# Performance work log

Hardware: AMD Instinct MI355X
Metric: run time of the kernel (lower is better)

Reference implementation:

```python
import jax, jax.numpy as jnp
import numpy as np
from jax import lax

B, T, E, H, V, D_ACT, OUT = 128, 512, 12, 512, 16, 10, 64


def setup_inputs() -> dict:
    key = jax.random.key(0)
    ks = jax.random.split(key, 9)
    ts = jax.random.uniform(ks[0], (B, T, 2), dtype=jnp.float32)
    idx = jax.random.randint(ks[1], (B, T), 0, V).astype(jnp.float32)
    x = jnp.concatenate([ts, idx[..., None]], axis=-1)  # [B,T,3], col2 = activity ids
    emb = jax.random.normal(ks[2], (V, D_ACT), jnp.float32) * 0.1
    emb = emb.at[0].set(0.0)  # padding_idx=0
    W_fwd = jax.random.normal(ks[3], (E, 3 * H), jnp.float32) / np.sqrt(E).astype(np.float32)
    b_fwd = jnp.zeros((3 * H,), jnp.float32)
    W_bwd = jax.random.normal(ks[4], (E, 3 * H), jnp.float32) / np.sqrt(E).astype(np.float32)
    b_bwd = jnp.zeros((3 * H,), jnp.float32)
    weight_Mu = jax.random.normal(ks[5], (2 * H, 1), jnp.float32) * 0.1
    W_out = jax.random.normal(ks[6], (OUT, 2 * H), jnp.float32) * 0.01  # torch Linear layout [out,in]
    b_out = jnp.zeros((OUT,), jnp.float32)
    return {"x": x, "emb": emb, "W_fwd": W_fwd, "b_fwd": b_fwd,
            "W_bwd": W_bwd, "b_bwd": b_bwd, "weight_Mu": weight_Mu,
            "W_out": W_out, "b_out": b_out}


def _fo_pool(z, f):
    # h_t = f_t * h_{t-1} + (1 - f_t) * z_t, scanned over time (axis 0)
    def step(c, zf):
        z_t, f_t = zf
        c = f_t * c + (1.0 - f_t) * z_t
        return c, c
    c0 = jnp.zeros_like(z[0])
    _, cs = lax.scan(step, c0, (z, f))
    return cs  # [T,B,H]


def _qrnn_dir(inp, W, b):
    # inp: [T,B,E] -> gates [T,B,3H]
    Y = inp @ W + b
    Z, F_, O = jnp.split(Y, 3, axis=-1)
    Z = jnp.tanh(Z)
    F_ = jax.nn.sigmoid(F_)
    O = jax.nn.sigmoid(O)
    C = _fo_pool(Z, F_)
    return O * C  # [T,B,H]


def reference(x, emb, W_fwd, b_fwd, W_bwd, b_bwd, weight_Mu, W_out, b_out):
    ts = x[:, :, :2]                                   # [B,T,2] time features
    act = emb[x[:, :, 2].astype(jnp.int32)]            # [B,T,10]
    enc = jnp.concatenate([ts, act], axis=-1)          # [B,T,E]
    inp = jnp.transpose(enc, (1, 0, 2))                # [T,B,E]
    h_f = _qrnn_dir(inp, W_fwd, b_fwd)                 # [T,B,H]
    h_b = _qrnn_dir(inp[::-1], W_bwd, b_bwd)[::-1]     # reverse-direction QRNN
    out = jnp.concatenate([h_f, h_b], axis=-1)         # [T,B,2H]
    out = jax.nn.relu(jnp.transpose(out, (1, 0, 2)))   # [B,T,2H]
    attn = jax.nn.softmax(out @ weight_Mu, axis=1)     # [B,T,1], softmax over time
    context = jnp.einsum('btd,bt->bd', out, attn[..., 0])  # [B,2H]
    context = jax.nn.relu(context)
    return context @ W_out.T + b_out                   # [B,OUT]
```

## Files before the change

kernel.cpp:

```cpp
#include <hip/hip_runtime.h>
#include <hip/hip_bf16.h>

typedef short short8 __attribute__((ext_vector_type(8)));

#define B_   128
#define T_   512
#define H_   512
#define V_   16
#define OUT_ 64
#define DH_  1024

#define SCAN_LDS (V_*H_*16 + T_*16)

__device__ __forceinline__ float bf2f(unsigned short u) {
    union { unsigned int i; float f; } x; x.i = ((unsigned int)u) << 16; return x.f;
}
__device__ __forceinline__ float sigm(float x) {
    return __builtin_amdgcn_rcpf(1.f + __expf(-x));
}

__global__ __launch_bounds__(512) void qrnn_scan2(
    const float* __restrict__ x,
    const float* __restrict__ emb,
    const float* __restrict__ Wf, const float* __restrict__ bf_,
    const float* __restrict__ Wb, const float* __restrict__ bb_,
    __hip_bfloat16* __restrict__ hbuf)
{
    const int b = blockIdx.x, dir = blockIdx.y, h = threadIdx.x;
    const float* __restrict__ W    = dir ? Wb  : Wf;
    const float* __restrict__ bias = dir ? bb_ : bf_;

    extern __shared__ char smem[];
    float4* tab = (float4*)smem;
    float4* tsq = (float4*)(smem + V_*H_*16);

    {
        const int t = h;
        const float* xp = x + ((size_t)b*T_ + t)*3;
        float t0 = xp[0], t1 = xp[1];
        int v = (int)xp[2];
        tsq[t] = make_float4(t0, t1, __int_as_float(v), 0.f);
    }

    float w0[3], w1[3], wt[10][3];
#pragma unroll
    for (int g = 0; g < 3; ++g) {
        w0[g] = W[g*H_ + h];
        w1[g] = W[1536 + g*H_ + h];
#pragma unroll
        for (int e = 0; e < 10; ++e)
            wt[e][g] = W[(2+e)*1536 + g*H_ + h];
    }
    const float bz = bias[h], bfv = bias[H_+h], bov = bias[2*H_+h];

#pragma unroll
    for (int v = 0; v < V_; ++v) {
        float a0 = bz, a1 = bfv, a2 = bov;
#pragma unroll
        for (int e = 0; e < 10; ++e) {
            const float ev = emb[v*10 + e];
            a0 = fmaf(ev, wt[e][0], a0);
            a1 = fmaf(ev, wt[e][1], a1);
            a2 = fmaf(ev, wt[e][2], a2);
        }
        tab[v*H_ + h] = make_float4(a0, a1, a2, 0.f);
    }
    __syncthreads();

    float c = 0.f;
    __hip_bfloat16* hb = hbuf + ((size_t)b*T_ + (dir ? T_-1 : 0))*DH_ + dir*H_ + h;
    const ptrdiff_t stride = dir ? -(ptrdiff_t)DH_ : (ptrdiff_t)DH_;
    int t = dir ? T_-1 : 0;
    const int tstep = dir ? -1 : 1;

#pragma unroll 4
    for (int s = 0; s < T_; ++s) {
        const float4 q = tsq[t];
        const int v = __float_as_int(q.z);
        const float4 g = tab[v*H_ + h];
        float zp = fmaf(q.x, w0[0], fmaf(q.y, w1[0], g.x));
        float fp = fmaf(q.x, w0[1], fmaf(q.y, w1[1], g.y));
        float op = fmaf(q.x, w0[2], fmaf(q.y, w1[2], g.z));
        const float f = sigm(fp);
        const float o = sigm(op);
        const float z = fmaf(2.f, sigm(2.f*zp), -1.f);
        c = fmaf(f, c - z, z);
        const float hv = fmaxf(o * c, 0.f);
        *hb = __float2bfloat16(hv);
        hb += stride; t += tstep;
    }
}

__global__ __launch_bounds__(256) void score2(
    const __hip_bfloat16* __restrict__ hbuf, const float* __restrict__ Mu,
    float* __restrict__ s)
{
    const int row  = blockIdx.x*4 + (threadIdx.x >> 6);
    const int lane = threadIdx.x & 63;
    const short8* hp = (const short8*)(hbuf + (size_t)row*DH_);
    const float4* mp = (const float4*)Mu;
    float acc = 0.f;
#pragma unroll
    for (int k = 0; k < 2; ++k) {
        const int idx = k*64 + lane;
        const short8 hv = hp[idx];
        const float4 m0 = mp[idx*2];
        const float4 m1 = mp[idx*2 + 1];
        acc = fmaf(bf2f((unsigned short)hv[0]), m0.x, acc);
        acc = fmaf(bf2f((unsigned short)hv[1]), m0.y, acc);
        acc = fmaf(bf2f((unsigned short)hv[2]), m0.z, acc);
        acc = fmaf(bf2f((unsigned short)hv[3]), m0.w, acc);
        acc = fmaf(bf2f((unsigned short)hv[4]), m1.x, acc);
        acc = fmaf(bf2f((unsigned short)hv[5]), m1.y, acc);
        acc = fmaf(bf2f((unsigned short)hv[6]), m1.z, acc);
        acc = fmaf(bf2f((unsigned short)hv[7]), m1.w, acc);
    }
#pragma unroll
    for (int off = 32; off; off >>= 1) acc += __shfl_down(acc, off);
    if (lane == 0) s[row] = acc;
}

__global__ __launch_bounds__(512) void softmax_kernel(
    const float* __restrict__ s, float* __restrict__ w)
{
    const int b = blockIdx.x;
    const int t = threadIdx.x;
    const float v = s[b*T_ + t];

    __shared__ float redm[8];
    __shared__ float reds[8];

    float m = v;
#pragma unroll
    for (int off = 32; off; off >>= 1) m = fmaxf(m, __shfl_xor(m, off));
    if ((t & 63) == 0) redm[t >> 6] = m;
    __syncthreads();
    float mall = redm[0];
#pragma unroll
    for (int i = 1; i < 8; ++i) mall = fmaxf(mall, redm[i]);

    const float e = __expf(v - mall);
    float sum = e;
#pragma unroll
    for (int off = 32; off; off >>= 1) sum += __shfl_xor(sum, off);
    if ((t & 63) == 0) reds[t >> 6] = sum;
    __syncthreads();
    float sall = 0.f;
#pragma unroll
    for (int i = 0; i < 8; ++i) sall += reds[i];

    w[b*T_ + t] = e / sall;
}

__global__ __launch_bounds__(256) void context2(
    const __hip_bfloat16* __restrict__ hbuf, const float* __restrict__ w,
    float* __restrict__ ctx)
{
    const int b  = blockIdx.x;
    const int d0 = (blockIdx.y*256 + threadIdx.x)*2;

    __shared__ float ws[T_];
    for (int t = threadIdx.x; t < T_; t += 256) ws[t] = w[b*T_ + t];
    __syncthreads();

    const unsigned int* hp = (const unsigned int*)(hbuf + (size_t)b*T_*DH_ + d0);
    float a0 = 0.f, a1 = 0.f;
#pragma unroll 8
    for (int t = 0; t < T_; ++t) {
        const unsigned int u = hp[(size_t)t*(DH_/2)];
        a0 = fmaf(bf2f((unsigned short)(u & 0xffffu)), ws[t], a0);
        a1 = fmaf(bf2f((unsigned short)(u >> 16)),     ws[t], a1);
    }
    float2* cp = (float2*)(ctx + b*DH_ + d0);
    *cp = make_float2(fmaxf(a0, 0.f), fmaxf(a1, 0.f));
}

__global__ __launch_bounds__(256) void out_kernel(
    const float* __restrict__ ctx, const float* __restrict__ Wout,
    const float* __restrict__ bout, float* __restrict__ out)
{
    const int idx  = blockIdx.x*4 + (threadIdx.x >> 6);
    const int lane = threadIdx.x & 63;
    const int b = idx >> 6;
    const int o = idx & 63;
    const float* cp = ctx + b*DH_;
    const float* wp = Wout + o*DH_;
    float acc = 0.f;
#pragma unroll
    for (int k = 0; k < DH_/64; ++k) {
        const int d = lane + k*64;
        acc = fmaf(cp[d], wp[d], acc);
    }
#pragma unroll
    for (int off = 32; off; off >>= 1) acc += __shfl_down(acc, off);
    if (lane == 0) out[idx] = acc + bout[o];
}

extern "C" void kernel_launch(void* const* d_in, const int* in_sizes, int n_in,
                              void* d_out, int out_size, void* d_ws, size_t ws_size,
                              hipStream_t stream)
{
    const float* x    = (const float*)d_in[0];
    const float* emb  = (const float*)d_in[1];
    const float* Wf   = (const float*)d_in[2];
    const float* bf_  = (const float*)d_in[3];
    const float* Wb   = (const float*)d_in[4];
    const float* bb_  = (const float*)d_in[5];
    const float* Mu   = (const float*)d_in[6];
    const float* Wout = (const float*)d_in[7];
    const float* bout = (const float*)d_in[8];
    float* out = (float*)d_out;

    char* ws = (char*)d_ws;
    const size_t hbytes = (size_t)B_*T_*DH_*sizeof(__hip_bfloat16);
    __hip_bfloat16* hbuf = (__hip_bfloat16*)ws;
    float* s   = (float*)(ws + hbytes);
    float* w   = s + B_*T_;
    float* ctx = w + B_*T_;

    (void)hipFuncSetAttribute((const void*)qrnn_scan2,
                              hipFuncAttributeMaxDynamicSharedMemorySize,
                              SCAN_LDS);

    qrnn_scan2<<<dim3(B_, 2), 512, SCAN_LDS, stream>>>(x, emb, Wf, bf_, Wb, bb_, hbuf);
    score2<<<(B_*T_)/4, 256, 0, stream>>>(hbuf, Mu, s);
    softmax_kernel<<<B_, 512, 0, stream>>>(s, w);
    context2<<<dim3(B_, 2), 256, 0, stream>>>(hbuf, w, ctx);
    out_kernel<<<(B_*OUT_)/4, 256, 0, stream>>>(ctx, Wout, bout, out);
}
```

Measured before the change: 209.7 us.

## Fuse attention score into QRNN scan and split context reduction over time

Each scan step now computes the attention score on the fly: the wave reduces h·Mu with shuffles and atomically adds it into the score buffer, so the separate score kernel and its full re-read of hbuf go away. The scan reads timestep features and vocab ids in packed 8-step groups to cut LDS loads. The context kernel is split into 8 time chunks per batch with atomic accumulation, and the ReLU moves into the output kernel. A zero kernel clears the accumulators first. In exchange, every step now pays for six shuffles plus atomics inside the serial scan loop.

After: 296.4 us. 41.4% more time.

```diff
diff --git a/kernel.cpp b/kernel.cpp
--- a/kernel.cpp
+++ b/kernel.cpp
@@ -1,7 +1,5 @@
 #include <hip/hip_runtime.h>
 #include <hip/hip_bf16.h>
-
-typedef short short8 __attribute__((ext_vector_type(8)));
 
 #define B_   128
 #define T_   512
@@ -10,7 +8,10 @@
 #define OUT_ 64
 #define DH_  1024
 
-#define SCAN_LDS (V_*H_*16 + T_*16)
+#define TAB_BYTES (V_*H_*16)
+#define TSA_BYTES (T_*8)
+#define VPK_BYTES (T_)
+#define SCAN_LDS  (TAB_BYTES + TSA_BYTES + VPK_BYTES)
 
 __device__ __forceinline__ float bf2f(unsigned short u) {
     union { unsigned int i; float f; } x; x.i = ((unsigned int)u) << 16; return x.f;
@@ -19,27 +20,36 @@
     return __builtin_amdgcn_rcpf(1.f + __expf(-x));
 }
 
-__global__ __launch_bounds__(512) void qrnn_scan2(
+__global__ __launch_bounds__(256) void zero_kernel(float4* __restrict__ p, int n4)
+{
+    const int i = blockIdx.x * 256 + threadIdx.x;
+    if (i < n4) p[i] = make_float4(0.f, 0.f, 0.f, 0.f);
+}
+
+__global__ __launch_bounds__(512) void qrnn_scan3(
     const float* __restrict__ x,
     const float* __restrict__ emb,
     const float* __restrict__ Wf, const float* __restrict__ bf_,
     const float* __restrict__ Wb, const float* __restrict__ bb_,
-    __hip_bfloat16* __restrict__ hbuf)
+    const float* __restrict__ Mu,
+    __hip_bfloat16* __restrict__ hbuf,
+    float* __restrict__ s)
 {
     const int b = blockIdx.x, dir = blockIdx.y, h = threadIdx.x;
+    const int lane = h & 63;
     const float* __restrict__ W    = dir ? Wb  : Wf;
     const float* __restrict__ bias = dir ? bb_ : bf_;
 
     extern __shared__ char smem[];
-    float4* tab = (float4*)smem;
-    float4* tsq = (float4*)(smem + V_*H_*16);
+    float4*        tab = (float4*)smem;
+    float2*        tsA = (float2*)(smem + TAB_BYTES);
+    unsigned char* vpk = (unsigned char*)(smem + TAB_BYTES + TSA_BYTES);
 
     {
         const int t = h;
         const float* xp = x + ((size_t)b*T_ + t)*3;
-        float t0 = xp[0], t1 = xp[1];
-        int v = (int)xp[2];
-        tsq[t] = make_float4(t0, t1, __int_as_float(v), 0.f);
+        tsA[t] = make_float2(xp[0], xp[1]);
+        vpk[t] = (unsigned char)(int)xp[2];
     }
 
     float w0[3], w1[3], wt[10][3];
@@ -65,59 +75,71 @@
         }
         tab[v*H_ + h] = make_float4(a0, a1, a2, 0.f);
     }
-    __syncthreads();
+    const float mu = Mu[dir*H_ + h];
+    __syncthreads();
+
+    const float4* tsA4 = (const float4*)tsA;
+    const uint2*  vp2  = (const uint2*)vpk;
 
     float c = 0.f;
-    __hip_bfloat16* hb = hbuf + ((size_t)b*T_ + (dir ? T_-1 : 0))*DH_ + dir*H_ + h;
-    const ptrdiff_t stride = dir ? -(ptrdiff_t)DH_ : (ptrdiff_t)DH_;
-    int t = dir ? T_-1 : 0;
-    const int tstep = dir ? -1 : 1;
-
-#pragma unroll 4
-    for (int s = 0; s < T_; ++s) {
-        const float4 q = tsq[t];
-        const int v = __float_as_int(q.z);
-        const float4 g = tab[v*H_ + h];
-        float zp = fmaf(q.x, w0[0], fmaf(q.y, w1[0], g.x));
-        float fp = fmaf(q.x, w0[1], fmaf(q.y, w1[1], g.y));
-        float op = fmaf(q.x, w0[2], fmaf(q.y, w1[2], g.z));
-        const float f = sigm(fp);
-        const float o = sigm(op);
-        const float z = fmaf(2.f, sigm(2.f*zp), -1.f);
-        c = fmaf(f, c - z, z);
-        const float hv = fmaxf(o * c, 0.f);
-        *hb = __float2bfloat16(hv);
-        hb += stride; t += tstep;
-    }
-}
-
-__global__ __launch_bounds__(256) void score2(
-    const __hip_bfloat16* __restrict__ hbuf, const float* __restrict__ Mu,
-    float* __restrict__ s)
-{
-    const int row  = blockIdx.x*4 + (threadIdx.x >> 6);
-    const int lane = threadIdx.x & 63;
-    const short8* hp = (const short8*)(hbuf + (size_t)row*DH_);
-    const float4* mp = (const float4*)Mu;
-    float acc = 0.f;
-#pragma unroll
-    for (int k = 0; k < 2; ++k) {
-        const int idx = k*64 + lane;
-        const short8 hv = hp[idx];
-        const float4 m0 = mp[idx*2];
-        const float4 m1 = mp[idx*2 + 1];
-        acc = fmaf(bf2f((unsigned short)hv[0]), m0.x, acc);
-        acc = fmaf(bf2f((unsigned short)hv[1]), m0.y, acc);
-        acc = fmaf(bf2f((unsigned short)hv[2]), m0.z, acc);
-        acc = fmaf(bf2f((unsigned short)hv[3]), m0.w, acc);
-        acc = fmaf(bf2f((unsigned short)hv[4]), m1.x, acc);
-        acc = fmaf(bf2f((unsigned short)hv[5]), m1.y, acc);
-        acc = fmaf(bf2f((unsigned short)hv[6]), m1.z, acc);
-        acc = fmaf(bf2f((unsigned short)hv[7]), m1.w, acc);
-    }
-#pragma unroll
-    for (int off = 32; off; off >>= 1) acc += __shfl_down(acc, off);
-    if (lane == 0) s[row] = acc;
+    __hip_bfloat16* hb = hbuf + (size_t)b*T_*DH_ + dir*H_ + h;
+    float* sb = s + b*T_;
+
+#define STEP(i, TS0, TS1, G) { \
+    const int t = t0 + (i); \
+    float zp = fmaf(TS0, w0[0], fmaf(TS1, w1[0], (G).x)); \
+    float fp = fmaf(TS0, w0[1], fmaf(TS1, w1[1], (G).y)); \
+    float op = fmaf(TS0, w0[2], fmaf(TS1, w1[2], (G).z)); \
+    const float f = sigm(fp); \
+    const float o = sigm(op); \
+    const float z = fmaf(2.f, sigm(2.f*zp), -1.f); \
+    c = fmaf(f, c - z, z); \
+    const float hv = fmaxf(o * c, 0.f); \
+    hb[(size_t)t*DH_] = __float2bfloat16(hv); \
+    float red = hv * mu; \
+    red += __shfl_xor(red, 1); \
+    red += __shfl_xor(red, 2); \
+    red += __shfl_xor(red, 4); \
+    red += __shfl_xor(red, 8); \
+    red += __shfl_xor(red, 16); \
+    red += __shfl_xor(red, 32); \
+    if (lane == 0) atomicAdd(&sb[t], red); \
+}
+
+#pragma unroll 2
+    for (int gi = 0; gi < T_/8; ++gi) {
+        const int gg = dir ? (T_/8 - 1 - gi) : gi;
+        const int t0 = gg*8;
+        const uint2  vp  = vp2[gg];
+        const float4 tsa = tsA4[gg*4 + 0];
+        const float4 tsb = tsA4[gg*4 + 1];
+        const float4 tsc = tsA4[gg*4 + 2];
+        const float4 tsd = tsA4[gg*4 + 3];
+        const int v0 =  vp.x        & 255, v1 = (vp.x >> 8) & 255;
+        const int v2 = (vp.x >> 16) & 255, v3 =  vp.x >> 24;
+        const int v4 =  vp.y        & 255, v5 = (vp.y >> 8) & 255;
+        const int v6 = (vp.y >> 16) & 255, v7 =  vp.y >> 24;
+        const float4 g0 = tab[v0*H_ + h];
+        const float4 g1 = tab[v1*H_ + h];
+        const float4 g2 = tab[v2*H_ + h];
+        const float4 g3 = tab[v3*H_ + h];
+        const float4 g4 = tab[v4*H_ + h];
+        const float4 g5 = tab[v5*H_ + h];
+        const float4 g6 = tab[v6*H_ + h];
+        const float4 g7 = tab[v7*H_ + h];
+        if (dir == 0) {
+            STEP(0, tsa.x, tsa.y, g0) STEP(1, tsa.z, tsa.w, g1)
+            STEP(2, tsb.x, tsb.y, g2) STEP(3, tsb.z, tsb.w, g3)
+            STEP(4, tsc.x, tsc.y, g4) STEP(5, tsc.z, tsc.w, g5)
+            STEP(6, tsd.x, tsd.y, g6) STEP(7, tsd.z, tsd.w, g7)
+        } else {
+            STEP(7, tsd.z, tsd.w, g7) STEP(6, tsd.x, tsd.y, g6)
+            STEP(5, tsc.z, tsc.w, g5) STEP(4, tsc.x, tsc.y, g4)
+            STEP(3, tsb.z, tsb.w, g3) STEP(2, tsb.x, tsb.y, g2)
+            STEP(1, tsa.z, tsa.w, g1) STEP(0, tsa.x, tsa.y, g0)
+        }
+    }
+#undef STEP
 }
 
 __global__ __launch_bounds__(512) void softmax_kernel(
@@ -152,27 +174,33 @@
     w[b*T_ + t] = e / sall;
 }
 
-__global__ __launch_bounds__(256) void context2(
+__global__ __launch_bounds__(256) void context3(
     const __hip_bfloat16* __restrict__ hbuf, const float* __restrict__ w,
     float* __restrict__ ctx)
 {
-    const int b  = blockIdx.x;
-    const int d0 = (blockIdx.y*256 + threadIdx.x)*2;
-
-    __shared__ float ws[T_];
-    for (int t = threadIdx.x; t < T_; t += 256) ws[t] = w[b*T_ + t];
-    __syncthreads();
-
-    const unsigned int* hp = (const unsigned int*)(hbuf + (size_t)b*T_*DH_ + d0);
-    float a0 = 0.f, a1 = 0.f;
+    const int b = blockIdx.x, q = blockIdx.y;
+    const int d0 = threadIdx.x * 4;
+
+    __shared__ float ws[64];
+    if (threadIdx.x < 64) ws[threadIdx.x] = w[b*T_ + q*64 + threadIdx.x];
+    __syncthreads();
+
+    const char* hp = (const char*)(hbuf + ((size_t)b*T_ + q*64)*DH_ + d0);
+    float a0 = 0.f, a1 = 0.f, a2 = 0.f, a3 = 0.f;
 #pragma unroll 8
-    for (int t = 0; t < T_; ++t) {
-        const unsigned int u = hp[(size_t)t*(DH_/2)];
-        a0 = fmaf(bf2f((unsigned short)(u & 0xffffu)), ws[t], a0);
-        a1 = fmaf(bf2f((unsigned short)(u >> 16)),     ws[t], a1);
-    }
-    float2* cp = (float2*)(ctx + b*DH_ + d0);
-    *cp = make_float2(fmaxf(a0, 0.f), fmaxf(a1, 0.f));
+    for (int i = 0; i < 64; ++i) {
+        const uint2 u = *(const uint2*)(hp + (size_t)i*(DH_*2));
+        const float wv = ws[i];
+        a0 = fmaf(bf2f((unsigned short)(u.x & 0xffffu)), wv, a0);
+        a1 = fmaf(bf2f((unsigned short)(u.x >> 16)),     wv, a1);
+        a2 = fmaf(bf2f((unsigned short)(u.y & 0xffffu)), wv, a2);
+        a3 = fmaf(bf2f((unsigned short)(u.y >> 16)),     wv, a3);
+    }
+    float* cp = ctx + b*DH_ + d0;
+    atomicAdd(cp + 0, a0);
+    atomicAdd(cp + 1, a1);
+    atomicAdd(cp + 2, a2);
+    atomicAdd(cp + 3, a3);
 }
 
 __global__ __launch_bounds__(256) void out_kernel(
@@ -189,7 +217,7 @@
 #pragma unroll
     for (int k = 0; k < DH_/64; ++k) {
         const int d = lane + k*64;
-        acc = fmaf(cp[d], wp[d], acc);
+        acc = fmaf(fmaxf(cp[d], 0.f), wp[d], acc);
     }
 #pragma unroll
     for (int off = 32; off; off >>= 1) acc += __shfl_down(acc, off);
@@ -218,13 +246,16 @@
     float* w   = s + B_*T_;
     float* ctx = w + B_*T_;
 
-    (void)hipFuncSetAttribute((const void*)qrnn_scan2,
+    (void)hipFuncSetAttribute((const void*)qrnn_scan3,
                               hipFuncAttributeMaxDynamicSharedMemorySize,
                               SCAN_LDS);
 
-    qrnn_scan2<<<dim3(B_, 2), 512, SCAN_LDS, stream>>>(x, emb, Wf, bf_, Wb, bb_, hbuf);
-    score2<<<(B_*T_)/4, 256, 0, stream>>>(hbuf, Mu, s);
+    const int n4 = (2*B_*T_ + B_*DH_) / 4;
+    zero_kernel<<<(n4 + 255)/256, 256, 0, stream>>>((float4*)s, n4);
+
+    qrnn_scan3<<<dim3(B_, 2), 512, SCAN_LDS, stream>>>(x, emb, Wf, bf_, Wb, bb_,
+                                                       Mu, hbuf, s);
     softmax_kernel<<<B_, 512, 0, stream>>>(s, w);
-    context2<<<dim3(B_, 2), 256, 0, stream>>>(hbuf, w, ctx);
+    context3<<<dim3(B_, 8), 256, 0, stream>>>(hbuf, w, ctx);
     out_kernel<<<(B_*OUT_)/4, 256, 0, stream>>>(ctx, Wout, bout, out);
 }
```
